# Performance work log

Hardware: AMD Instinct MI355X
Metric: run time of the kernel (lower is better)

The kernel has to match this reference:

```python
import jax, jax.numpy as jnp
import numpy as np

B, CIN, H, W = 32, 64, 112, 112
COUT, KH, KW = 64, 3, 3
STRIDE = (1, 1)
PADDING = ((1, 1), (1, 1))
DILATION = (1, 1)


def setup_inputs() -> dict:
    key = jax.random.key(0)
    k1, k2, k3 = jax.random.split(key, 3)
    # quantized activations and weights, int8 value range [-128, 127]
    x_q = jax.random.randint(k1, (B, CIN, H, W), -128, 128, dtype=jnp.int32).astype(jnp.int8)
    w_q = jax.random.randint(k2, (COUT, CIN, KH, KW), -128, 128, dtype=jnp.int32).astype(jnp.int8)
    weight_scale = jnp.float32(0.02)   # per-tensor weight scale
    act_scale = jnp.float32(0.05)      # per-tensor activation scale
    bias = jax.random.normal(k3, (COUT,), dtype=jnp.float32)
    return {"x_q": x_q, "w_q": w_q, "weight_scale": weight_scale,
            "act_scale": act_scale, "bias": bias}


def reference(x_q, w_q, weight_scale, act_scale, bias):
    acc = jax.lax.conv_general_dilated(
        x_q.astype(jnp.int32), w_q.astype(jnp.int32),
        window_strides=STRIDE, padding=PADDING, rhs_dilation=DILATION,
        dimension_numbers=("NCHW", "OIHW", "NCHW"),
        preferred_element_type=jnp.int32)
    # fused dequant (per-tensor scales) + FP32 bias -> FP32 output [B, COUT, H, W]
    out = acc.astype(jnp.float32) * (act_scale * weight_scale) + bias[None, :, None, None]
    return out
```

## Files before the change

### kernel.cpp

```cpp
#include <hip/hip_runtime.h>
#include <stdint.h>

#define BATCH 32
#define CIN   64
#define HH    112
#define WW    112
#define COUT_ 64

typedef int v4i __attribute__((ext_vector_type(4)));

#define WT_OFF   0
#define ZP_OFF   36864
#define XT_OFF   65536
#define XT_NEED  (65536 + 26167296)

__global__ void wtrans_kernel(const int* __restrict__ wq, int8_t* __restrict__ wt) {
    int idx = blockIdx.x * 256 + threadIdx.x;
    int ci   = idx & 63;
    int khkw = (idx >> 6) % 9;
    int co   = idx / 576;
    wt[idx] = (int8_t)wq[co * 576 + ci * 9 + khkw];
}

__global__ void xtrans_kernel(const int* __restrict__ x, int8_t* __restrict__ ws) {
    int8_t* __restrict__ xt = ws + XT_OFF;
    const int bid = blockIdx.x;
    const int tid = threadIdx.x;
    if (bid < 6272) {
        int idx  = bid * 256 + tid;
        int ci4  = idx & 15;
        int rest = idx >> 4;
        int cg   = rest % 28;
        int bh   = rest / 28;
        int h    = bh % 112;
        int b    = bh / 112;
        const v4i* gp = (const v4i*)(x + ((b * CIN + ci4 * 4) * HH + h) * WW + cg * 4);
        v4i q0 = gp[0];
        v4i q1 = gp[3136];
        v4i q2 = gp[2 * 3136];
        v4i q3 = gp[3 * 3136];
        int8_t* rowp = xt + (size_t)bh * 114 * 64;
        #pragma unroll
        for (int j = 0; j < 4; ++j) {
            uint32_t lo01 = __builtin_amdgcn_perm((uint32_t)q1[j], (uint32_t)q0[j], 0x0C0C0400u);
            uint32_t lo23 = __builtin_amdgcn_perm((uint32_t)q3[j], (uint32_t)q2[j], 0x04000C0Cu);
            int col = cg * 4 + 1 + j;
            int sd  = (((ci4 >> 2) ^ (col & 3)) << 2) | (ci4 & 3);
            *(uint32_t*)&rowp[col * 64 + sd * 4] = lo01 | lo23;
        }
    } else if (bid < 6720) {
        int idx  = (bid - 6272) * 256 + tid;
        int d    = idx & 15;
        int side = (idx >> 4) & 1;
        int bh   = idx >> 5;
        int col  = side ? 113 : 0;
        *(uint32_t*)&xt[((size_t)bh * 114 + col) * 64 + d * 4] = 0u;
    } else {
        int idx = (bid - 6720) * 256 + tid;
        if (idx < 1824) *(uint32_t*)&ws[ZP_OFF + idx * 4] = 0u;
    }
}

__launch_bounds__(256, 3)
__global__ void conv2_kernel(const int8_t* __restrict__ ws,
                             const float*  __restrict__ wscale,
                             const float*  __restrict__ ascale,
                             const float*  __restrict__ bias,
                             float*        __restrict__ out) {
    __shared__ int8_t xs[4 * 114 * 64];

    const int tid = threadIdx.x;
    const int bt  = blockIdx.x;
    const int b   = bt / 56;
    const int h0  = (bt % 56) * 2;

    const int8_t* __restrict__ xt = ws + XT_OFF;
    const int8_t* __restrict__ zp = ws + ZP_OFF;
    const int8_t* __restrict__ wt = ws + WT_OFF;

    const int8_t* srow[4];
    #pragma unroll
    for (int r = 0; r < 4; ++r) {
        int hh = h0 - 1 + r;
        srow[r] = (hh >= 0 && hh < HH) ? xt + (size_t)(b * HH + hh) * 114 * 64 : zp;
    }
    #pragma unroll
    for (int i = 0; i < 8; ++i) {
        int idx = tid + i * 256;
        if (idx < 1824) {
            int row = idx / 456;
            int rem = idx - row * 456;
            __builtin_amdgcn_global_load_lds(
                (const __attribute__((address_space(1))) int*)(srow[row] + rem * 16),
                (__attribute__((address_space(3))) int*)(&xs[idx * 16]),
                16, 0, 0);
        }
    }
    __syncthreads();

    const int lane = tid & 63;
    const int wave = tid >> 6;
    const int ln15 = lane & 15;
    const int quad = lane >> 4;

    const v4i* wrow = (const v4i*)(wt + (size_t)(wave * 16 + ln15) * 576);
    v4i a[9];
    #pragma unroll
    for (int t = 0; t < 9; ++t) a[t] = wrow[t * 4 + quad];

    v4i acc[2][7];
    #pragma unroll
    for (int r = 0; r < 2; ++r)
        #pragma unroll
        for (int nt = 0; nt < 7; ++nt)
            acc[r][nt] = (v4i){0, 0, 0, 0};

    #pragma unroll
    for (int tap = 0; tap < 9; ++tap) {
        const int kh = tap / 3;
        const int kw = tap % 3;
        const int swz = (quad ^ ((ln15 + kw) & 3)) << 4;
        #pragma unroll
        for (int r = 0; r < 2; ++r) {
            const int8_t* bp = &xs[((kh + r) * 114 + ln15 + kw) * 64 + swz];
            #pragma unroll
            for (int nt = 0; nt < 7; ++nt) {
                v4i bfrag = *(const v4i*)(bp + nt * 1024);
                acc[r][nt] = __builtin_amdgcn_mfma_i32_16x16x64_i8(a[tap], bfrag, acc[r][nt], 0, 0, 0);
            }
        }
    }

    const float s = ascale[0] * wscale[0];
    #pragma unroll
    for (int r = 0; r < 2; ++r) {
        const int h = h0 + r;
        #pragma unroll
        for (int reg = 0; reg < 4; ++reg) {
            int co = wave * 16 + quad * 4 + reg;
            float bv = bias[co];
            float* op = out + ((size_t)(b * COUT_ + co) * HH + h) * WW;
            #pragma unroll
            for (int nt = 0; nt < 7; ++nt)
                op[nt * 16 + ln15] = (float)acc[r][nt][reg] * s + bv;
        }
    }
}

__launch_bounds__(256, 2)
__global__ void conv_kernel(const int* __restrict__ x,
                            const int8_t* __restrict__ wt,
                            const float*  __restrict__ wscale,
                            const float*  __restrict__ ascale,
                            const float*  __restrict__ bias,
                            float*        __restrict__ out) {
    __shared__ int8_t xs[4 * 114 * 72];

    const int tid = threadIdx.x;
    const int bt  = blockIdx.x;
    const int b   = bt / 56;
    const int h0  = (bt % 56) * 2;

    #pragma unroll
    for (int it = 0; it < 7; ++it) {
        int job = tid + it * 256;
        int ci4 = job & 15;
        int cg  = (job >> 4) % 28;
        int row = job / 448;
        int hh  = h0 - 1 + row;
        v4i q0 = {0,0,0,0}, q1 = {0,0,0,0}, q2 = {0,0,0,0}, q3 = {0,0,0,0};
        if (hh >= 0 && hh < HH) {
            const v4i* gp = (const v4i*)
                (x + ((size_t)(b * CIN + ci4 * 4) * HH + hh) * WW + cg * 4);
            q0 = gp[0];
            q1 = gp[3136];
            q2 = gp[2 * 3136];
            q3 = gp[3 * 3136];
        }
        #pragma unroll
        for (int j = 0; j < 4; ++j) {
            uint32_t lo01 = __builtin_amdgcn_perm((uint32_t)q1[j], (uint32_t)q0[j], 0x0C0C0400u);
            uint32_t lo23 = __builtin_amdgcn_perm((uint32_t)q3[j], (uint32_t)q2[j], 0x04000C0Cu);
            int addr = (row * 114 + cg * 4 + 1 + j) * 72 + ci4 * 4;
            *(uint32_t*)&xs[addr] = lo01 | lo23;
        }
    }
    if (tid < 128) {
        int ci4 = tid & 15;
        int col = ((tid >> 4) & 1) ? 113 : 0;
        int row = tid >> 5;
        *(uint32_t*)&xs[(row * 114 + col) * 72 + ci4 * 4] = 0u;
    }
    __syncthreads();

    const int lane = tid & 63;
    const int wave = tid >> 6;
    const int ln15 = lane & 15;
    const int quad = lane >> 4;
    const int r    = wave >> 1;
    const int coh  = wave & 1;
    const int cobase = coh * 32;

    v4i acc[2][7];
    #pragma unroll
    for (int mt = 0; mt < 2; ++mt)
        #pragma unroll
        for (int nt = 0; nt < 7; ++nt)
            acc[mt][nt] = (v4i){0, 0, 0, 0};

    const long* w64a = (const long*)(wt + (size_t)(cobase + ln15) * 576);
    const long* w64b = (const long*)(wt + (size_t)(cobase + 16 + ln15) * 576);

    #pragma unroll
    for (int kc = 0; kc < 18; ++kc) {
        const int khkw = kc >> 1;
        const int kh   = khkw / 3;
        const int kw   = khkw % 3;
        const int half = kc & 1;
        long a0 = w64a[kc * 4 + quad];
        long a1 = w64b[kc * 4 + quad];
        const int rowb  = (kh + r) * 114;
        const int cioff = half * 32 + quad * 8;
        #pragma unroll
        for (int nt = 0; nt < 7; ++nt) {
            int col = nt * 16 + ln15 + kw;
            long bfrag = *(const long*)&xs[(rowb + col) * 72 + cioff];
            acc[0][nt] = __builtin_amdgcn_mfma_i32_16x16x32_i8(a0, bfrag, acc[0][nt], 0, 0, 0);
            acc[1][nt] = __builtin_amdgcn_mfma_i32_16x16x32_i8(a1, bfrag, acc[1][nt], 0, 0, 0);
        }
    }

    const float s = ascale[0] * wscale[0];
    const int h = h0 + r;
    #pragma unroll
    for (int mt = 0; mt < 2; ++mt) {
        #pragma unroll
        for (int reg = 0; reg < 4; ++reg) {
            int co = cobase + mt * 16 + quad * 4 + reg;
            float bv = bias[co];
            float* op = out + ((size_t)(b * COUT_ + co) * HH + h) * WW;
            #pragma unroll
            for (int nt = 0; nt < 7; ++nt) {
                int wp = nt * 16 + ln15;
                op[wp] = (float)acc[mt][nt][reg] * s + bv;
            }
        }
    }
}

extern "C" void kernel_launch(void* const* d_in, const int* in_sizes, int n_in,
                              void* d_out, int out_size, void* d_ws, size_t ws_size,
                              hipStream_t stream) {
    const int*    xq     = (const int*)d_in[0];
    const int*    wq     = (const int*)d_in[1];
    const float*  wscale = (const float*)d_in[2];
    const float*  ascale = (const float*)d_in[3];
    const float*  bias   = (const float*)d_in[4];
    int8_t* ws  = (int8_t*)d_ws;
    float*  out = (float*)d_out;

    wtrans_kernel<<<144, 256, 0, stream>>>(wq, ws);
    if (ws_size >= (size_t)XT_NEED) {
        xtrans_kernel<<<6728, 256, 0, stream>>>(xq, ws);
        conv2_kernel<<<BATCH * 56, 256, 0, stream>>>(ws, wscale, ascale, bias, out);
    } else {
        conv_kernel<<<BATCH * 56, 256, 0, stream>>>(xq, ws, wscale, ascale, bias, out);
    }
}
```

Baseline: 222.8 us.

## Reuse LDS B-fragments across both output rows and change swizzle pattern

Reorders the conv inner loop by input row so each LDS-loaded activation fragment feeds MFMAs for both output rows, reducing LDS reads by a third. Changes the XOR swizzle of the transposed activation layout to key on column pairs, aiming to lower LDS bank conflicts for the 16-byte fragment loads. Also computes global_load_lds source addresses inline instead of via a pointer array. The producer and consumer swizzles must match, which they do here.

```diff
diff --git a/kernel.cpp b/kernel.cpp
--- a/kernel.cpp
+++ b/kernel.cpp
@@ -45,7 +45,7 @@
             uint32_t lo01 = __builtin_amdgcn_perm((uint32_t)q1[j], (uint32_t)q0[j], 0x0C0C0400u);
             uint32_t lo23 = __builtin_amdgcn_perm((uint32_t)q3[j], (uint32_t)q2[j], 0x04000C0Cu);
             int col = cg * 4 + 1 + j;
-            int sd  = (((ci4 >> 2) ^ (col & 3)) << 2) | (ci4 & 3);
+            int sd  = (((ci4 >> 2) ^ ((col >> 1) & 3)) << 2) | (ci4 & 3);
             *(uint32_t*)&rowp[col * 64 + sd * 4] = lo01 | lo23;
         }
     } else if (bid < 6720) {
@@ -78,20 +78,18 @@
     const int8_t* __restrict__ zp = ws + ZP_OFF;
     const int8_t* __restrict__ wt = ws + WT_OFF;
 
-    const int8_t* srow[4];
-    #pragma unroll
-    for (int r = 0; r < 4; ++r) {
-        int hh = h0 - 1 + r;
-        srow[r] = (hh >= 0 && hh < HH) ? xt + (size_t)(b * HH + hh) * 114 * 64 : zp;
-    }
     #pragma unroll
     for (int i = 0; i < 8; ++i) {
         int idx = tid + i * 256;
         if (idx < 1824) {
             int row = idx / 456;
             int rem = idx - row * 456;
+            int hh  = h0 - 1 + row;
+            const int8_t* src = (hh >= 0 && hh < HH)
+                ? xt + ((size_t)(b * HH + hh) * 7296 + rem * 16)
+                : zp + rem * 16;
             __builtin_amdgcn_global_load_lds(
-                (const __attribute__((address_space(1))) int*)(srow[row] + rem * 16),
+                (const __attribute__((address_space(1))) int*)src,
                 (__attribute__((address_space(3))) int*)(&xs[idx * 16]),
                 16, 0, 0);
         }
@@ -116,17 +114,21 @@
             acc[r][nt] = (v4i){0, 0, 0, 0};
 
     #pragma unroll
-    for (int tap = 0; tap < 9; ++tap) {
-        const int kh = tap / 3;
-        const int kw = tap % 3;
-        const int swz = (quad ^ ((ln15 + kw) & 3)) << 4;
-        #pragma unroll
-        for (int r = 0; r < 2; ++r) {
-            const int8_t* bp = &xs[((kh + r) * 114 + ln15 + kw) * 64 + swz];
+    for (int rho = 0; rho < 4; ++rho) {
+        #pragma unroll
+        for (int kw = 0; kw < 3; ++kw) {
+            const int m   = ln15 + kw;
+            const int swz = (quad ^ ((m >> 1) & 3)) << 4;
+            const int8_t* bp = &xs[(rho * 114 + m) * 64 + swz];
             #pragma unroll
             for (int nt = 0; nt < 7; ++nt) {
                 v4i bfrag = *(const v4i*)(bp + nt * 1024);
-                acc[r][nt] = __builtin_amdgcn_mfma_i32_16x16x64_i8(a[tap], bfrag, acc[r][nt], 0, 0, 0);
+                if (rho <= 2)
+                    acc[0][nt] = __builtin_amdgcn_mfma_i32_16x16x64_i8(
+                        a[rho * 3 + kw], bfrag, acc[0][nt], 0, 0, 0);
+                if (rho >= 1)
+                    acc[1][nt] = __builtin_amdgcn_mfma_i32_16x16x64_i8(
+                        a[(rho - 1) * 3 + kw], bfrag, acc[1][nt], 0, 0, 0);
             }
         }
     }
```

Result: faster. 209.7 us (-5.9%).
